# Optimization experiments

Hardware: AMD Instinct MI355X
Metric: run time of the kernel (lower is better)

## Reference

```python
import jax, jax.numpy as jnp
import numpy as np

N_INST, BATCH, IN_DIM, L_DIM = 256, 128, 1024, 512

def setup_inputs() -> dict:
    key = jax.random.key(0)
    k1, k2, k3, k4 = jax.random.split(key, 4)
    # glorot-uniform-ish scales
    sv = np.sqrt(6.0 / (IN_DIM + L_DIM)).astype(np.float32)
    sw = np.sqrt(6.0 / (L_DIM + 1)).astype(np.float32)
    x = jax.random.normal(k1, (N_INST, BATCH, IN_DIM), dtype=jnp.float32)
    v = jax.random.uniform(k2, (IN_DIM, L_DIM), minval=-sv, maxval=sv, dtype=jnp.float32)
    u = jax.random.uniform(k3, (IN_DIM, L_DIM), minval=-sv, maxval=sv, dtype=jnp.float32)
    w = jax.random.uniform(k4, (L_DIM, 1), minval=-sw, maxval=sw, dtype=jnp.float32)
    return {"x": x, "v": v, "u": u, "w": w}

def reference(x, v, u, w):
    # x: [n_instances, batch, in_dim]
    # Fused batched version of the per-instance loop:
    # score_i = (tanh(x_i @ v) * sigmoid(x_i @ u)) @ w, softmax over instances.
    h = jnp.tanh(jnp.einsum('nbd,dl->nbl', x, v))          # [n, b, l]
    g = jax.nn.sigmoid(jnp.einsum('nbd,dl->nbl', x, u))    # [n, b, l]
    scores = jnp.einsum('nbl,lo->nbo', h * g, w)            # [n, b, 1]
    alpha = jax.nn.softmax(scores, axis=0)                  # softmax over instance axis
    return alpha
```

## Files before the change

kernel.cpp:

```cpp
#include <hip/hip_runtime.h>
#include <stdint.h>

typedef unsigned int  u32;
typedef unsigned short u16;
typedef __bf16 v8bf __attribute__((ext_vector_type(8)));
typedef float  v4f  __attribute__((ext_vector_type(4)));

#define N_INST 256
#define BATCH  128
#define IN_DIM 1024
#define L_DIM  512
#define M_TOT  (N_INST*BATCH)

#define BM 128
#define BN 128
#define BK 64
#define KITERS (IN_DIM/BK)
#define NSLICE 16

#define XB_BYTES   ((size_t)M_TOT * IN_DIM * 2)
#define WPK_BYTES  ((size_t)1024 * IN_DIM * 2)

__device__ inline u32 f2bf_pk(float a, float b){
  u32 ua = __builtin_bit_cast(u32, a);
  u32 ub = __builtin_bit_cast(u32, b);
  ua = (ua + 0x7FFFu + ((ua >> 16) & 1u)) >> 16;
  ub = (ub + 0x7FFFu + ((ub >> 16) & 1u)) & 0xFFFF0000u;
  return ua | ub;
}

#define PREP_XBLKS 16384
__global__ void prep(const float* __restrict__ x, const float* __restrict__ v,
                     const float* __restrict__ u, u16* __restrict__ xb,
                     u16* __restrict__ wpk){
  const int b = blockIdx.x;
  if (b < PREP_XBLKS){
    int t = b * 256 + threadIdx.x;
    int r = t >> 6, l = t & 63;
    int kk = r & 1, i = (r >> 1) & 3, h = (r >> 3) & 1, kt = (r >> 4) & 15, mb = r >> 8;
    int q = l >> 4, c = l & 15;
    int row = mb*128 + h*64 + i*16 + c;
    int k0  = kt*64 + kk*32 + q*8;
    const float* src = x + (size_t)row * IN_DIM + k0;
    float4 a0 = *reinterpret_cast<const float4*>(src);
    float4 a1 = *reinterpret_cast<const float4*>(src + 4);
    uint4 out;
    out.x = f2bf_pk(a0.x, a0.y); out.y = f2bf_pk(a0.z, a0.w);
    out.z = f2bf_pk(a1.x, a1.y); out.w = f2bf_pk(a1.z, a1.w);
    *reinterpret_cast<uint4*>(xb + (size_t)r*512 + l*8) = out;
  } else {
    int t = (b - PREP_XBLKS) * 256 + threadIdx.x;
    int r = t >> 6, l = t & 63;
    int kk = r & 1, j = (r >> 1) & 3, h = (r >> 3) & 1, kt = (r >> 4) & 15, nb = r >> 8;
    int q = l >> 4, c = l & 15;
    int bcol = nb*8 + h*4 + j;
    const float* src = (bcol & 1) ? u : v;
    int lcol = (bcol >> 1)*16 + c;
    int k0 = kt*64 + kk*32 + q*8;
    u32 o[4];
#pragma unroll
    for (int ii = 0; ii < 4; ++ii){
      float a  = src[(size_t)(k0 + 2*ii    ) * L_DIM + lcol];
      float bb = src[(size_t)(k0 + 2*ii + 1) * L_DIM + lcol];
      o[ii] = f2bf_pk(a, bb);
    }
    *reinterpret_cast<uint4*>(wpk + (size_t)r*512 + l*8) = make_uint4(o[0], o[1], o[2], o[3]);
  }
}

__launch_bounds__(256)
__global__ void gemm_score(const u16* __restrict__ xb, const u16* __restrict__ wpk,
                           const float* __restrict__ w, float* __restrict__ partial){
  const int tid  = threadIdx.x;
  const u32 bid  = blockIdx.x;
  const int xcd  = bid & 7;
  const int slot = bid >> 3;
  const int nblk = slot & 7;
  const int mblk = xcd * 32 + (slot >> 3);
  const int m0   = mblk * BM;

  const int lane = tid & 63;
  const int wave = tid >> 6;
  const int ha   = wave >> 1;
  const int hb   = wave & 1;
  const int q    = lane >> 4;
  const int c    = lane & 15;

  const u16* pa = xb  + (size_t)mblk*131072 + ha*4096 + lane*8;
  const u16* pb = wpk + (size_t)nblk*131072 + hb*4096 + lane*8;

  v4f acc[4][4];
#pragma unroll
  for (int i = 0; i < 4; ++i)
#pragma unroll
    for (int j = 0; j < 4; ++j)
      acc[i][j] = (v4f){0.f, 0.f, 0.f, 0.f};

#pragma unroll 1
  for (int kt = 0; kt < KITERS; ++kt){
    const u16* a = pa + kt*8192;
    const u16* b = pb + kt*8192;
    v8bf af[8], bfr[8];
#pragma unroll
    for (int f = 0; f < 8; ++f){
      af[f]  = *reinterpret_cast<const v8bf*>(a + f*512);
      bfr[f] = *reinterpret_cast<const v8bf*>(b + f*512);
    }
#pragma unroll
    for (int kk = 0; kk < 2; ++kk)
#pragma unroll
      for (int i = 0; i < 4; ++i)
#pragma unroll
        for (int j = 0; j < 4; ++j)
          acc[i][j] = __builtin_amdgcn_mfma_f32_16x16x32_bf16(af[i*2+kk], bfr[j*2+kk], acc[i][j], 0, 0, 0);
  }

  const int lbase = nblk*64 + hb*32 + c;
  const float wl0 = w[lbase];
  const float wl1 = w[lbase + 16];
  const int p = nblk*2 + hb;
  float* pout = partial + (size_t)p * M_TOT + m0 + ha*64;

#pragma unroll
  for (int i = 0; i < 4; ++i){
#pragma unroll
    for (int r = 0; r < 4; ++r){
      float t0 = 2.f / (1.f + __expf(-2.f * acc[i][0][r])) - 1.f;
      float s0 = 1.f / (1.f + __expf(-acc[i][1][r]));
      float t1 = 2.f / (1.f + __expf(-2.f * acc[i][2][r])) - 1.f;
      float s1 = 1.f / (1.f + __expf(-acc[i][3][r]));
      float v2 = t0*s0*wl0 + t1*s1*wl1;
      v2 += __shfl_xor(v2, 1, 64);
      v2 += __shfl_xor(v2, 2, 64);
      v2 += __shfl_xor(v2, 4, 64);
      v2 += __shfl_xor(v2, 8, 64);
      if (c == 0) pout[i*16 + q*4 + r] = v2;
    }
  }
}

__global__ void softmax_inst(const float* __restrict__ partial, float* __restrict__ out){
  __shared__ float red[N_INST];
  const int b = blockIdx.x;
  const int n = threadIdx.x;
  float s = 0.f;
#pragma unroll
  for (int i = 0; i < NSLICE; ++i) s += partial[(size_t)i * M_TOT + n*BATCH + b];
  red[n] = s; __syncthreads();
  for (int st = N_INST/2; st > 0; st >>= 1){
    if (n < st) red[n] = fmaxf(red[n], red[n + st]);
    __syncthreads();
  }
  float mx = red[0]; __syncthreads();
  float e = __expf(s - mx);
  red[n] = e; __syncthreads();
  for (int st = N_INST/2; st > 0; st >>= 1){
    if (n < st) red[n] += red[n + st];
    __syncthreads();
  }
  out[n*BATCH + b] = e / red[0];
}

extern "C" void kernel_launch(void* const* d_in, const int* in_sizes, int n_in,
                              void* d_out, int out_size, void* d_ws, size_t ws_size,
                              hipStream_t stream) {
  const float* x = (const float*)d_in[0];
  const float* v = (const float*)d_in[1];
  const float* u = (const float*)d_in[2];
  const float* w = (const float*)d_in[3];
  u16*   xb      = (u16*)d_ws;
  u16*   wpk     = (u16*)((char*)d_ws + XB_BYTES);
  float* partial = (float*)((char*)d_ws + XB_BYTES + WPK_BYTES);
  float* out     = (float*)d_out;

  prep<<<dim3(PREP_XBLKS + 512), dim3(256), 0, stream>>>(x, v, u, xb, wpk);
  gemm_score<<<dim3(2048), dim3(256), 0, stream>>>(xb, wpk, w, partial);
  softmax_inst<<<dim3(BATCH), dim3(N_INST), 0, stream>>>(partial, out);
}
```

Baseline: 303.4 us.

## Stage weight slice in LDS and compute 512x32 tiles per block

Each block now owns a 32-column slice of the fused v/u weights, staged into 64KB of shared memory with global_load_lds in two K halves. The block covers four 128-row M blocks, so the B operand is reused from LDS across them instead of being re-read from global memory for every tile. The weight packing is reorganised to match, and the grid is halved to 1024 blocks with launch bounds requesting 2 blocks per CU. The cost is mid-loop barriers for restaging B, A fragments still loaded straight from global memory, and higher register and LDS use that may limit occupancy.

```diff
diff --git a/kernel.cpp b/kernel.cpp
--- a/kernel.cpp
+++ b/kernel.cpp
@@ -11,11 +11,6 @@
 #define IN_DIM 1024
 #define L_DIM  512
 #define M_TOT  (N_INST*BATCH)
-
-#define BM 128
-#define BN 128
-#define BK 64
-#define KITERS (IN_DIM/BK)
 #define NSLICE 16
 
 #define XB_BYTES   ((size_t)M_TOT * IN_DIM * 2)
@@ -27,6 +22,12 @@
   ua = (ua + 0x7FFFu + ((ua >> 16) & 1u)) >> 16;
   ub = (ub + 0x7FFFu + ((ub >> 16) & 1u)) & 0xFFFF0000u;
   return ua | ub;
+}
+
+__device__ inline void gl2lds16(const u16* g, u16* l){
+  __builtin_amdgcn_global_load_lds(
+      (const __attribute__((address_space(1))) u32*)(g),
+      (__attribute__((address_space(3))) u32*)(l), 16, 0, 0);
 }
 
 #define PREP_XBLKS 16384
@@ -51,9 +52,9 @@
   } else {
     int t = (b - PREP_XBLKS) * 256 + threadIdx.x;
     int r = t >> 6, l = t & 63;
-    int kk = r & 1, j = (r >> 1) & 3, h = (r >> 3) & 1, kt = (r >> 4) & 15, nb = r >> 8;
+    int kk = r & 1, j = (r >> 1) & 3, kt = (r >> 3) & 15, cs = r >> 7;
     int q = l >> 4, c = l & 15;
-    int bcol = nb*8 + h*4 + j;
+    int bcol = cs*4 + j;
     const float* src = (bcol & 1) ? u : v;
     int lcol = (bcol >> 1)*16 + c;
     int k0 = kt*64 + kk*32 + q*8;
@@ -68,73 +69,107 @@
   }
 }
 
-__launch_bounds__(256)
+__launch_bounds__(256, 2)
 __global__ void gemm_score(const u16* __restrict__ xb, const u16* __restrict__ wpk,
                            const float* __restrict__ w, float* __restrict__ partial){
+  __shared__ __align__(16) u16 Bs[64 * 512];
+
   const int tid  = threadIdx.x;
   const u32 bid  = blockIdx.x;
   const int xcd  = bid & 7;
   const int slot = bid >> 3;
-  const int nblk = slot & 7;
-  const int mblk = xcd * 32 + (slot >> 3);
-  const int m0   = mblk * BM;
+  const int cs   = slot & 15;
+  const int mr   = xcd*8 + (slot >> 4);
+  const int mblk0= mr * 4;
 
   const int lane = tid & 63;
   const int wave = tid >> 6;
-  const int ha   = wave >> 1;
-  const int hb   = wave & 1;
   const int q    = lane >> 4;
   const int c    = lane & 15;
 
-  const u16* pa = xb  + (size_t)mblk*131072 + ha*4096 + lane*8;
-  const u16* pb = wpk + (size_t)nblk*131072 + hb*4096 + lane*8;
-
-  v4f acc[4][4];
-#pragma unroll
-  for (int i = 0; i < 4; ++i)
-#pragma unroll
-    for (int j = 0; j < 4; ++j)
-      acc[i][j] = (v4f){0.f, 0.f, 0.f, 0.f};
+  auto stageB = [&](int kh){
+    const u16* src = wpk + (size_t)(cs*128 + kh*64) * 512;
+#pragma unroll
+    for (int it = 0; it < 16; ++it){
+      const int rl = wave*16 + it;
+      gl2lds16(src + (size_t)rl*512 + lane*8, &Bs[rl*512 + lane*8]);
+    }
+  };
+
+  const u16* awave = xb + (size_t)mblk0*131072 + (size_t)(2*wave)*1024 + lane*8;
+
+  v4f acc[4][2][4];
+#pragma unroll
+  for (int mb = 0; mb < 4; ++mb)
+#pragma unroll
+    for (int gi = 0; gi < 2; ++gi)
+#pragma unroll
+      for (int j = 0; j < 4; ++j)
+        acc[mb][gi][j] = (v4f){0.f, 0.f, 0.f, 0.f};
+
+  stageB(0);
+  __syncthreads();
 
 #pragma unroll 1
-  for (int kt = 0; kt < KITERS; ++kt){
-    const u16* a = pa + kt*8192;
-    const u16* b = pb + kt*8192;
-    v8bf af[8], bfr[8];
-#pragma unroll
-    for (int f = 0; f < 8; ++f){
-      af[f]  = *reinterpret_cast<const v8bf*>(a + f*512);
-      bfr[f] = *reinterpret_cast<const v8bf*>(b + f*512);
-    }
-#pragma unroll
-    for (int kk = 0; kk < 2; ++kk)
-#pragma unroll
-      for (int i = 0; i < 4; ++i)
-#pragma unroll
-        for (int j = 0; j < 4; ++j)
-          acc[i][j] = __builtin_amdgcn_mfma_f32_16x16x32_bf16(af[i*2+kk], bfr[j*2+kk], acc[i][j], 0, 0, 0);
-  }
-
-  const int lbase = nblk*64 + hb*32 + c;
-  const float wl0 = w[lbase];
-  const float wl1 = w[lbase + 16];
-  const int p = nblk*2 + hb;
-  float* pout = partial + (size_t)p * M_TOT + m0 + ha*64;
-
-#pragma unroll
-  for (int i = 0; i < 4; ++i){
-#pragma unroll
-    for (int r = 0; r < 4; ++r){
-      float t0 = 2.f / (1.f + __expf(-2.f * acc[i][0][r])) - 1.f;
-      float s0 = 1.f / (1.f + __expf(-acc[i][1][r]));
-      float t1 = 2.f / (1.f + __expf(-2.f * acc[i][2][r])) - 1.f;
-      float s1 = 1.f / (1.f + __expf(-acc[i][3][r]));
-      float v2 = t0*s0*wl0 + t1*s1*wl1;
-      v2 += __shfl_xor(v2, 1, 64);
-      v2 += __shfl_xor(v2, 2, 64);
-      v2 += __shfl_xor(v2, 4, 64);
-      v2 += __shfl_xor(v2, 8, 64);
-      if (c == 0) pout[i*16 + q*4 + r] = v2;
+  for (int kh = 0; kh < 2; ++kh){
+#pragma unroll 1
+    for (int ktl = 0; ktl < 8; ++ktl){
+      const int kt = kh*8 + ktl;
+      v8bf bfr[4][2];
+#pragma unroll
+      for (int j = 0; j < 4; ++j)
+#pragma unroll
+        for (int kk = 0; kk < 2; ++kk)
+          bfr[j][kk] = *reinterpret_cast<const v8bf*>(&Bs[(ktl*8 + j*2 + kk)*512 + lane*8]);
+      v8bf af[4][2][2];
+      const u16* ak = awave + (size_t)kt * 8192;
+#pragma unroll
+      for (int mb = 0; mb < 4; ++mb)
+#pragma unroll
+        for (int gi = 0; gi < 2; ++gi)
+#pragma unroll
+          for (int kk = 0; kk < 2; ++kk)
+            af[mb][gi][kk] = *reinterpret_cast<const v8bf*>(ak + mb*131072 + gi*1024 + kk*512);
+#pragma unroll
+      for (int mb = 0; mb < 4; ++mb)
+#pragma unroll
+        for (int kk = 0; kk < 2; ++kk)
+#pragma unroll
+          for (int gi = 0; gi < 2; ++gi)
+#pragma unroll
+            for (int j = 0; j < 4; ++j)
+              acc[mb][gi][j] = __builtin_amdgcn_mfma_f32_16x16x32_bf16(
+                  af[mb][gi][kk], bfr[j][kk], acc[mb][gi][j], 0, 0, 0);
+    }
+    if (kh == 0){
+      __syncthreads();
+      stageB(1);
+      __syncthreads();
+    }
+  }
+
+  const float wl0 = w[cs*32 + c];
+  const float wl1 = w[cs*32 + 16 + c];
+  float* pbase = partial + (size_t)cs * M_TOT;
+
+#pragma unroll
+  for (int mb = 0; mb < 4; ++mb){
+    float* pout = pbase + (size_t)(mblk0 + mb)*128 + wave*32;
+#pragma unroll
+    for (int gi = 0; gi < 2; ++gi){
+#pragma unroll
+      for (int r = 0; r < 4; ++r){
+        float t0 = 2.f / (1.f + __expf(-2.f * acc[mb][gi][0][r])) - 1.f;
+        float s0 = 1.f / (1.f + __expf(-acc[mb][gi][1][r]));
+        float t1 = 2.f / (1.f + __expf(-2.f * acc[mb][gi][2][r])) - 1.f;
+        float s1 = 1.f / (1.f + __expf(-acc[mb][gi][3][r]));
+        float v2 = t0*s0*wl0 + t1*s1*wl1;
+        v2 += __shfl_xor(v2, 1, 64);
+        v2 += __shfl_xor(v2, 2, 64);
+        v2 += __shfl_xor(v2, 4, 64);
+        v2 += __shfl_xor(v2, 8, 64);
+        if (c == 0) pout[gi*16 + q*4 + r] = v2;
+      }
     }
   }
 }
@@ -174,6 +209,6 @@
   float* out     = (float*)d_out;
 
   prep<<<dim3(PREP_XBLKS + 512), dim3(256), 0, stream>>>(x, v, u, xb, wpk);
-  gemm_score<<<dim3(2048), dim3(256), 0, stream>>>(xb, wpk, w, partial);
+  gemm_score<<<dim3(1024), dim3(256), 0, stream>>>(xb, wpk, w, partial);
   softmax_inst<<<dim3(BATCH), dim3(N_INST), 0, stream>>>(partial, out);
 }
```

Result: slower. 320.9 us (+5.8%).
